# Optimization experiments

Hardware: AMD Instinct MI355X
Metric: run time of the kernel (lower is better)

Reference implementation:

```python
import jax, jax.numpy as jnp
import numpy as np

D_MODEL = 1024
N_HEADS = 16
D_K = D_MODEL // N_HEADS


def rotate_half(x):
    x1, x2 = x[..., : x.shape[-1] // 2], x[..., x.shape[-1] // 2:]
    return jnp.concatenate((-x2, x1), axis=-1)


def rope_cos_sin(seq_len, d_k, dtype):
    inv_freq = 1.0 / (10000.0 ** (jnp.arange(0, d_k, 2, dtype=jnp.float32) / d_k))
    t = jnp.arange(seq_len, dtype=jnp.float32)
    freqs = jnp.outer(t, inv_freq)            # [S, d_k/2]
    emb = jnp.concatenate((freqs, freqs), -1) # [S, d_k]
    return jnp.cos(emb).astype(dtype), jnp.sin(emb).astype(dtype)


def setup_inputs() -> dict:
    key = jax.random.key(0)
    ks = jax.random.split(key, 8)
    B, S = 1, 2048
    q = jax.random.normal(ks[0], (B, S, D_MODEL), jnp.float32)
    k = jax.random.normal(ks[1], (B, S, D_MODEL), jnp.float32)
    v = jax.random.normal(ks[2], (B, S, D_MODEL), jnp.float32)
    # xavier-uniform-ish weights for [d_model, d_model]
    bound = float(np.sqrt(6.0 / (D_MODEL + D_MODEL)))
    def W(kk):
        return jax.random.uniform(kk, (D_MODEL, D_MODEL), jnp.float32, -bound, bound)
    return {
        "query": q, "key": k, "value": v,
        "w_q": W(ks[3]), "w_k": W(ks[4]), "w_v": W(ks[5]),
        "w_o": W(ks[6]), "b_o": jnp.zeros((D_MODEL,), jnp.float32),
    }


def reference(query, key, value, w_q, w_k, w_v, w_o, b_o):
    B, Sq, _ = query.shape
    Sk = key.shape[1]
    # projections (torch Linear: x @ W.T)
    Q = (query @ w_q.T).reshape(B, Sq, N_HEADS, D_K).transpose(0, 2, 1, 3)
    K = (key @ w_k.T).reshape(B, Sk, N_HEADS, D_K).transpose(0, 2, 1, 3)
    V = (value @ w_v.T).reshape(B, Sk, N_HEADS, D_K).transpose(0, 2, 1, 3)
    # RoPE on Q and K (over head dim d_k)
    cos_q, sin_q = rope_cos_sin(Sq, D_K, Q.dtype)
    cos_k, sin_k = (cos_q, sin_q) if Sk == Sq else rope_cos_sin(Sk, D_K, K.dtype)
    Q = Q * cos_q + rotate_half(Q) * sin_q
    K = K * cos_k + rotate_half(K) * sin_k
    scores = jnp.einsum("bhqd,bhkd->bhqk", Q, K) / jnp.sqrt(jnp.float32(D_K)).astype(Q.dtype)
    attn = jax.nn.softmax(scores, axis=-1)          # [B,H,Sq,Sk]
    ctx = jnp.einsum("bhqk,bhkd->bhqd", attn, V)    # [B,H,Sq,d_k]
    ctx = ctx.transpose(0, 2, 1, 3).reshape(B, Sq, D_MODEL)
    out = ctx @ w_o.T + b_o
    return out, attn
```

## Files before the change

### kernel.cpp

```cpp
#include <hip/hip_runtime.h>
#include <hip/hip_bf16.h>

using short8 = __attribute__((ext_vector_type(8))) short;
using f32x4  = __attribute__((ext_vector_type(4))) float;

#define SEQ   2048
#define DM    1024
#define NHEAD 16
#define MB    1048576

#define GLD16(GP, LP) __builtin_amdgcn_global_load_lds(                      \
    (const __attribute__((address_space(1))) void*)(GP),                     \
    (__attribute__((address_space(3))) void*)(LP), 16, 0, 0)

static __device__ __forceinline__ short f2bf(float f) {
    union { __hip_bfloat16 b; short s; } u;
    u.b = __float2bfloat16(f);
    return u.s;
}
static __device__ __forceinline__ f32x4 mfma_bf16(short8 a, short8 b, f32x4 c) {
    return __builtin_amdgcn_mfma_f32_16x16x32_bf16(a, b, c, 0, 0, 0);
}

__global__ __launch_bounds__(256) void prep_kernel(
    const float* __restrict__ q, const float* __restrict__ k, const float* __restrict__ v,
    const float* __restrict__ wq, const float* __restrict__ wk, const float* __restrict__ wv,
    const float* __restrict__ wo, short* __restrict__ bf,
    float* __restrict__ cosT, float* __restrict__ sinT)
{
    long t = (long)blockIdx.x * 256 + threadIdx.x;
    if (t < 1310720) {
        long e0 = t * 8;
        const float* src; long off;
        if      (e0 < 2L*MB) { src = q;  off = e0; }
        else if (e0 < 4L*MB) { src = k;  off = e0 - 2L*MB; }
        else if (e0 < 6L*MB) { src = v;  off = e0 - 4L*MB; }
        else if (e0 < 7L*MB) { src = wq; off = e0 - 6L*MB; }
        else if (e0 < 8L*MB) { src = wk; off = e0 - 7L*MB; }
        else if (e0 < 9L*MB) { src = wv; off = e0 - 8L*MB; }
        else                 { src = wo; off = e0 - 9L*MB; }
        float4 a = *(const float4*)(src + off);
        float4 b = *(const float4*)(src + off + 4);
        short8 o;
        o[0]=f2bf(a.x); o[1]=f2bf(a.y); o[2]=f2bf(a.z); o[3]=f2bf(a.w);
        o[4]=f2bf(b.x); o[5]=f2bf(b.y); o[6]=f2bf(b.z); o[7]=f2bf(b.w);
        *(short8*)(bf + e0) = o;
    } else {
        long tt = t - 1310720;
        int s = (int)(tt >> 5), j = (int)(tt & 31);
        float invf = __expf(-(float)j * (9.210340371976184f / 32.0f));
        float arg = (float)s * invf;
        cosT[tt] = cosf(arg);
        sinT[tt] = sinf(arg);
    }
}

__global__ __launch_bounds__(256, 2) void gemm_qkv(
    short* __restrict__ wsbf, const float* __restrict__ cosT,
    const float* __restrict__ sinT)
{
    __shared__ short As[128 * 64];
    __shared__ short Bs[128 * 64];
    const int tid  = threadIdx.x;
    const int lane = tid & 63;
    const int wave = tid >> 6;
    const int q4   = lane >> 4;
    const int l16  = lane & 15;
    const int wm   = wave >> 1;
    const int wn   = wave & 1;
    const int m0   = blockIdx.y * 128;
    const int n0   = blockIdx.x * 128;
    const int z    = blockIdx.z;

    const short* A = wsbf + (size_t)z * (2*MB);
    const short* W = wsbf + 6*(size_t)MB + (size_t)z * MB;

    f32x4 zero = {0.f, 0.f, 0.f, 0.f};
    f32x4 acc[4][4];
    #pragma unroll
    for (int i = 0; i < 4; ++i)
        #pragma unroll
        for (int j = 0; j < 4; ++j) acc[i][j] = zero;

    const int r8 = tid >> 3, c8 = tid & 7;

    for (int k0 = 0; k0 < 1024; k0 += 64) {
        __syncthreads();
        #pragma unroll
        for (int r = 0; r < 4; ++r) {
            int row = r*32 + r8;
            int sw  = c8 ^ (row & 7);
            GLD16(A + (size_t)(m0+row)*1024 + k0 + sw*8, &As[(r*256 + tid)*8]);
            GLD16(W + (size_t)(n0+row)*1024 + k0 + sw*8, &Bs[(r*256 + tid)*8]);
        }
        __syncthreads();
        #pragma unroll
        for (int kk = 0; kk < 2; ++kk) {
            short8 af[4], bfr[4];
            #pragma unroll
            for (int i = 0; i < 4; ++i) {
                int ra = wm*64 + i*16 + l16;
                af[i]  = *(const short8*)&As[ra*64 + (((kk*4+q4) ^ (ra&7))*8)];
                int rb = wn*64 + i*16 + l16;
                bfr[i] = *(const short8*)&Bs[rb*64 + (((kk*4+q4) ^ (rb&7))*8)];
            }
            #pragma unroll
            for (int i = 0; i < 4; ++i)
                #pragma unroll
                for (int j = 0; j < 4; ++j)
                    acc[i][j] = mfma_bf16(af[i], bfr[j], acc[i][j]);
        }
    }

    const int h = (n0 >> 6) + wn;
    if (z < 2) {
        short* dst = wsbf + (size_t)(10 + 2*z) * MB;
        #pragma unroll
        for (int i = 0; i < 4; ++i) {
            #pragma unroll
            for (int jj = 0; jj < 4; ++jj) {
                int s = m0 + wm*64 + i*16 + q4*4 + jj;
                float c0 = cosT[(s<<5) + l16],      s0 = sinT[(s<<5) + l16];
                float c1 = cosT[(s<<5) + 16 + l16], s1 = sinT[(s<<5) + 16 + l16];
                float v0 = acc[i][0][jj], v1 = acc[i][1][jj];
                float v2 = acc[i][2][jj], v3 = acc[i][3][jj];
                size_t base = ((size_t)h*SEQ + s)*64;
                dst[base + l16]      = f2bf(v0*c0 - v2*s0);
                dst[base + 16 + l16] = f2bf(v1*c1 - v3*s1);
                dst[base + 32 + l16] = f2bf(v2*c0 + v0*s0);
                dst[base + 48 + l16] = f2bf(v3*c1 + v1*s1);
            }
        }
    } else {
        short* dst = wsbf + (size_t)14 * MB;
        #pragma unroll
        for (int i = 0; i < 4; ++i)
            #pragma unroll
            for (int j = 0; j < 4; ++j)
                #pragma unroll
                for (int jj = 0; jj < 4; ++jj) {
                    int s = m0 + wm*64 + i*16 + q4*4 + jj;
                    int d = j*16 + l16;
                    dst[((size_t)h*64 + d)*SEQ + s] = f2bf(acc[i][j][jj]);
                }
    }
}

__global__ __launch_bounds__(256, 2) void attn_kernel(
    const short* __restrict__ wsbf, short* __restrict__ ctxout,
    float* __restrict__ attn)
{
    __shared__ short Qs[64 * 64];
    __shared__ short Ks[2][128 * 64];
    __shared__ short Vs[64 * 128];
    __shared__ short Ps[4][16 * 128];
    const int tid = threadIdx.x, lane = tid & 63, wave = tid >> 6;
    const int q4 = lane >> 4, l16 = lane & 15;
    const int h = blockIdx.y, qt0 = blockIdx.x * 64;
    const short* Qg = wsbf + (size_t)10*MB + ((size_t)h*SEQ + qt0)*64;
    const short* Kg = wsbf + (size_t)12*MB + (size_t)h*SEQ*64;
    const short* Vg = wsbf + (size_t)14*MB + (size_t)h*64*SEQ;

    const int r8  = tid >> 3, c8  = tid & 7;
    const int r16 = tid >> 4, c16 = tid & 15;

    auto stageK = [&](int kt, short* buf) {
        #pragma unroll
        for (int r = 0; r < 4; ++r) {
            int row = r*32 + r8;
            int sw  = c8 ^ (row & 7);
            GLD16(Kg + (size_t)(kt*128 + row)*64 + sw*8, buf + (r*256 + tid)*8);
        }
    };
    auto stageV = [&](int kt) {
        #pragma unroll
        for (int r = 0; r < 4; ++r) {
            int row = r*16 + r16;
            int sw  = c16 ^ (row & 7);
            GLD16(Vg + (size_t)row*SEQ + kt*128 + sw*8, &Vs[(r*256 + tid)*8]);
        }
    };

    #pragma unroll
    for (int r = 0; r < 2; ++r) {
        int row = r*32 + r8;
        int sw  = c8 ^ (row & 7);
        GLD16(Qg + (size_t)row*64 + sw*8, &Qs[(r*256 + tid)*8]);
    }
    stageK(0, Ks[0]);
    __syncthreads();

    const int ra = wave*16 + l16;
    short8 a_q[2];
    #pragma unroll
    for (int kk = 0; kk < 2; ++kk)
        a_q[kk] = *(const short8*)&Qs[ra*64 + (((kk*4+q4) ^ (ra&7))*8)];

    f32x4 zero = {0.f, 0.f, 0.f, 0.f};
    f32x4 ctx[4] = {zero, zero, zero, zero};
    float rs[4] = {0.f, 0.f, 0.f, 0.f};
    const int frw = ((l16 & 7) + 2*(l16 >> 3)) & 7;

    for (int kt = 0; kt < 16; ++kt) {
        const short* Kb = (kt & 1) ? Ks[1] : Ks[0];
        short*       Kn = (kt & 1) ? Ks[0] : Ks[1];
        stageV(kt);
        if (kt < 15) stageK(kt + 1, Kn);
        #pragma unroll
        for (int nt = 0; nt < 8; ++nt) {
            f32x4 acc = zero;
            #pragma unroll
            for (int kk = 0; kk < 2; ++kk) {
                int rb = nt*16 + l16;
                short8 b = *(const short8*)&Kb[rb*64 + (((kk*4+q4) ^ (rb&7))*8)];
                acc = mfma_bf16(a_q[kk], b, acc);
            }
            #pragma unroll
            for (int jj = 0; jj < 4; ++jj) {
                float p = __expf(acc[jj] * 0.125f);
                rs[jj] += p;
                int prow = q4*4 + jj;
                int col  = nt*16 + l16;
                int fr   = ((prow & 7) + 2*(prow >> 3)) & 7;
                int phys = (col >> 3) ^ fr;
                Ps[wave][prow*128 + phys*8 + (col & 7)] = f2bf(p);
            }
        }
        if (kt < 15) asm volatile("s_waitcnt vmcnt(4) lgkmcnt(0)" ::: "memory");
        else         asm volatile("s_waitcnt vmcnt(0) lgkmcnt(0)" ::: "memory");
        __builtin_amdgcn_s_barrier();
        #pragma unroll
        for (int kks = 0; kks < 4; ++kks) {
            short8 a = *(const short8*)&Ps[wave][l16*128 + (((kks*4+q4) ^ frw)*8)];
            #pragma unroll
            for (int dt = 0; dt < 4; ++dt) {
                int rv = dt*16 + l16;
                short8 b = *(const short8*)&Vs[rv*128 + (((kks*4+q4) ^ (rv&7))*8)];
                ctx[dt] = mfma_bf16(a, b, ctx[dt]);
            }
        }
        asm volatile("s_waitcnt vmcnt(0) lgkmcnt(0)" ::: "memory");
        __builtin_amdgcn_s_barrier();
    }

    #pragma unroll
    for (int jj = 0; jj < 4; ++jj)
        #pragma unroll
        for (int m = 1; m < 16; m <<= 1)
            rs[jj] += __shfl_xor(rs[jj], m);
    float irs[4];
    #pragma unroll
    for (int jj = 0; jj < 4; ++jj) irs[jj] = 1.0f / rs[jj];

    const int qbase = qt0 + wave*16 + q4*4;
    #pragma unroll
    for (int dt = 0; dt < 4; ++dt)
        #pragma unroll
        for (int jj = 0; jj < 4; ++jj)
            ctxout[(size_t)(qbase + jj)*1024 + h*64 + dt*16 + l16] = f2bf(ctx[dt][jj] * irs[jj]);

    stageK(0, Ks[0]);
    asm volatile("s_waitcnt vmcnt(0) lgkmcnt(0)" ::: "memory");
    __builtin_amdgcn_s_barrier();

    float* arow = attn + (size_t)h*SEQ*SEQ;
    for (int kt = 0; kt < 16; ++kt) {
        const short* Kb = (kt & 1) ? Ks[1] : Ks[0];
        short*       Kn = (kt & 1) ? Ks[0] : Ks[1];
        if (kt < 15) stageK(kt + 1, Kn);
        #pragma unroll
        for (int nt = 0; nt < 8; ++nt) {
            f32x4 acc = zero;
            #pragma unroll
            for (int kk = 0; kk < 2; ++kk) {
                int rb = nt*16 + l16;
                short8 b = *(const short8*)&Kb[rb*64 + (((kk*4+q4) ^ (rb&7))*8)];
                acc = mfma_bf16(a_q[kk], b, acc);
            }
            #pragma unroll
            for (int jj = 0; jj < 4; ++jj)
                arow[(size_t)(qbase + jj)*SEQ + kt*128 + nt*16 + l16] =
                    __expf(acc[jj] * 0.125f) * irs[jj];
        }
        asm volatile("s_waitcnt vmcnt(32) lgkmcnt(0)" ::: "memory");
        __builtin_amdgcn_s_barrier();
    }
}

__global__ __launch_bounds__(256, 2) void gemm_out(
    const short* __restrict__ wsbf, const float* __restrict__ bo,
    float* __restrict__ out)
{
    __shared__ short As[128 * 64];
    __shared__ short Bs[64 * 64];
    const int tid = threadIdx.x, lane = tid & 63, wave = tid >> 6;
    const int q4 = lane >> 4, l16 = lane & 15;
    const int m0 = blockIdx.y * 128, n0 = blockIdx.x * 64;
    const short* A = wsbf + 16*(size_t)MB;
    const short* W = wsbf + 9*(size_t)MB;

    f32x4 zero = {0.f, 0.f, 0.f, 0.f};
    f32x4 acc[2][4];
    #pragma unroll
    for (int i = 0; i < 2; ++i)
        #pragma unroll
        for (int j = 0; j < 4; ++j) acc[i][j] = zero;

    const int r8 = tid >> 3, c8 = tid & 7;

    for (int k0 = 0; k0 < 1024; k0 += 64) {
        __syncthreads();
        #pragma unroll
        for (int r = 0; r < 4; ++r) {
            int row = r*32 + r8;
            int sw  = c8 ^ (row & 7);
            GLD16(A + (size_t)(m0+row)*1024 + k0 + sw*8, &As[(r*256 + tid)*8]);
        }
        #pragma unroll
        for (int r = 0; r < 2; ++r) {
            int row = r*32 + r8;
            int sw  = c8 ^ (row & 7);
            GLD16(W + (size_t)(n0+row)*1024 + k0 + sw*8, &Bs[(r*256 + tid)*8]);
        }
        __syncthreads();
        #pragma unroll
        for (int kk = 0; kk < 2; ++kk) {
            short8 af[2], bfr[4];
            #pragma unroll
            for (int i = 0; i < 2; ++i) {
                int ra = wave*32 + i*16 + l16;
                af[i] = *(const short8*)&As[ra*64 + (((kk*4+q4) ^ (ra&7))*8)];
            }
            #pragma unroll
            for (int j = 0; j < 4; ++j) {
                int rb = j*16 + l16;
                bfr[j] = *(const short8*)&Bs[rb*64 + (((kk*4+q4) ^ (rb&7))*8)];
            }
            #pragma unroll
            for (int i = 0; i < 2; ++i)
                #pragma unroll
                for (int j = 0; j < 4; ++j)
                    acc[i][j] = mfma_bf16(af[i], bfr[j], acc[i][j]);
        }
    }

    #pragma unroll
    for (int i = 0; i < 2; ++i)
        #pragma unroll
        for (int j = 0; j < 4; ++j)
            #pragma unroll
            for (int jj = 0; jj < 4; ++jj) {
                int gr = m0 + wave*32 + i*16 + q4*4 + jj;
                int gc = n0 + j*16 + l16;
                out[(size_t)gr*1024 + gc] = acc[i][j][jj] + bo[gc];
            }
}

extern "C" void kernel_launch(void* const* d_in, const int* in_sizes, int n_in,
                              void* d_out, int out_size, void* d_ws, size_t ws_size,
                              hipStream_t stream)
{
    const float* q  = (const float*)d_in[0];
    const float* k  = (const float*)d_in[1];
    const float* v  = (const float*)d_in[2];
    const float* wq = (const float*)d_in[3];
    const float* wk = (const float*)d_in[4];
    const float* wv = (const float*)d_in[5];
    const float* wo = (const float*)d_in[6];
    const float* bo = (const float*)d_in[7];

    short* wsbf = (short*)d_ws;
    float* cosT = (float*)((char*)d_ws + (size_t)36*MB);
    float* sinT = cosT + 65536;
    float* out  = (float*)d_out;
    float* attn = out + (size_t)SEQ*DM;

    hipLaunchKernelGGL(prep_kernel, dim3(5376), dim3(256), 0, stream,
                       q, k, v, wq, wk, wv, wo, wsbf, cosT, sinT);
    hipLaunchKernelGGL(gemm_qkv, dim3(8, 16, 3), dim3(256), 0, stream,
                       wsbf, cosT, sinT);
    hipLaunchKernelGGL(attn_kernel, dim3(32, 16), dim3(256), 0, stream,
                       wsbf, wsbf + (size_t)16*MB, attn);
    hipLaunchKernelGGL(gemm_out, dim3(16, 16), dim3(256), 0, stream,
                       wsbf, bo, out);
}
```

Before: 410.4 us.

## Double-buffer GEMM k-loops, keep P in registers, and vectorize attention-row stores

Both projection GEMMs now double-buffer their LDS tiles so the next k-slice loads while MFMAs run on the current one. The attention kernel swaps the MFMA operand order so each lane holds a transposed score tile. That lets the bf16 P fragments be packed straight from registers instead of round-tripping through an LDS scratch buffer, with V stored in a matching permuted sequence order. The attention-probability writeout becomes float4 stores per lane, and row sums are reduced with fewer shuffles. The cost is double the LDS in the GEMMs, which may reduce occupancy, plus more register pressure from holding P in the attention kernel.

New measurement: 389.2 us. -5.2%, faster.

```diff
diff --git a/kernel.cpp b/kernel.cpp
--- a/kernel.cpp
+++ b/kernel.cpp
@@ -59,8 +59,8 @@
     short* __restrict__ wsbf, const float* __restrict__ cosT,
     const float* __restrict__ sinT)
 {
-    __shared__ short As[128 * 64];
-    __shared__ short Bs[128 * 64];
+    __shared__ short As[2][128 * 64];
+    __shared__ short Bs[2][128 * 64];
     const int tid  = threadIdx.x;
     const int lane = tid & 63;
     const int wave = tid >> 6;
@@ -84,25 +84,33 @@
 
     const int r8 = tid >> 3, c8 = tid & 7;
 
-    for (int k0 = 0; k0 < 1024; k0 += 64) {
-        __syncthreads();
+    auto stage = [&](int k0, int buf) {
         #pragma unroll
         for (int r = 0; r < 4; ++r) {
             int row = r*32 + r8;
             int sw  = c8 ^ (row & 7);
-            GLD16(A + (size_t)(m0+row)*1024 + k0 + sw*8, &As[(r*256 + tid)*8]);
-            GLD16(W + (size_t)(n0+row)*1024 + k0 + sw*8, &Bs[(r*256 + tid)*8]);
-        }
-        __syncthreads();
+            GLD16(A + (size_t)(m0+row)*1024 + k0 + sw*8, &As[buf][(r*256 + tid)*8]);
+            GLD16(W + (size_t)(n0+row)*1024 + k0 + sw*8, &Bs[buf][(r*256 + tid)*8]);
+        }
+    };
+
+    stage(0, 0);
+    for (int t = 0; t < 16; ++t) {
+        if (t < 15) stage((t+1)*64, (t+1)&1);
+        if (t < 15) asm volatile("s_waitcnt vmcnt(8)" ::: "memory");
+        else        asm volatile("s_waitcnt vmcnt(0)" ::: "memory");
+        asm volatile("s_barrier" ::: "memory");
+        const short* as = As[t&1];
+        const short* bs = Bs[t&1];
         #pragma unroll
         for (int kk = 0; kk < 2; ++kk) {
             short8 af[4], bfr[4];
             #pragma unroll
             for (int i = 0; i < 4; ++i) {
                 int ra = wm*64 + i*16 + l16;
-                af[i]  = *(const short8*)&As[ra*64 + (((kk*4+q4) ^ (ra&7))*8)];
+                af[i]  = *(const short8*)&as[ra*64 + (((kk*4+q4) ^ (ra&7))*8)];
                 int rb = wn*64 + i*16 + l16;
-                bfr[i] = *(const short8*)&Bs[rb*64 + (((kk*4+q4) ^ (rb&7))*8)];
+                bfr[i] = *(const short8*)&bs[rb*64 + (((kk*4+q4) ^ (rb&7))*8)];
             }
             #pragma unroll
             for (int i = 0; i < 4; ++i)
@@ -110,6 +118,7 @@
                 for (int j = 0; j < 4; ++j)
                     acc[i][j] = mfma_bf16(af[i], bfr[j], acc[i][j]);
         }
+        asm volatile("s_barrier" ::: "memory");
     }
 
     const int h = (n0 >> 6) + wn;
@@ -139,9 +148,10 @@
             for (int j = 0; j < 4; ++j)
                 #pragma unroll
                 for (int jj = 0; jj < 4; ++jj) {
-                    int s = m0 + wm*64 + i*16 + q4*4 + jj;
-                    int d = j*16 + l16;
-                    dst[((size_t)h*64 + d)*SEQ + s] = f2bf(acc[i][j][jj]);
+                    int s  = m0 + wm*64 + i*16 + q4*4 + jj;
+                    int sp = (s & ~31) + q4*8 + (i&1)*4 + jj;
+                    int d  = j*16 + l16;
+                    dst[((size_t)h*64 + d)*SEQ + sp] = f2bf(acc[i][j][jj]);
                 }
     }
 }
@@ -153,7 +163,6 @@
     __shared__ short Qs[64 * 64];
     __shared__ short Ks[2][128 * 64];
     __shared__ short Vs[64 * 128];
-    __shared__ short Ps[4][16 * 128];
     const int tid = threadIdx.x, lane = tid & 63, wave = tid >> 6;
     const int q4 = lane >> 4, l16 = lane & 15;
     const int h = blockIdx.y, qt0 = blockIdx.x * 64;
@@ -198,14 +207,14 @@
 
     f32x4 zero = {0.f, 0.f, 0.f, 0.f};
     f32x4 ctx[4] = {zero, zero, zero, zero};
-    float rs[4] = {0.f, 0.f, 0.f, 0.f};
-    const int frw = ((l16 & 7) + 2*(l16 >> 3)) & 7;
+    float rsl = 0.f;
 
     for (int kt = 0; kt < 16; ++kt) {
         const short* Kb = (kt & 1) ? Ks[1] : Ks[0];
         short*       Kn = (kt & 1) ? Ks[0] : Ks[1];
         stageV(kt);
         if (kt < 15) stageK(kt + 1, Kn);
+        float p[8][4];
         #pragma unroll
         for (int nt = 0; nt < 8; ++nt) {
             f32x4 acc = zero;
@@ -213,44 +222,45 @@
             for (int kk = 0; kk < 2; ++kk) {
                 int rb = nt*16 + l16;
                 short8 b = *(const short8*)&Kb[rb*64 + (((kk*4+q4) ^ (rb&7))*8)];
-                acc = mfma_bf16(a_q[kk], b, acc);
+                acc = mfma_bf16(b, a_q[kk], acc);
             }
             #pragma unroll
             for (int jj = 0; jj < 4; ++jj) {
-                float p = __expf(acc[jj] * 0.125f);
-                rs[jj] += p;
-                int prow = q4*4 + jj;
-                int col  = nt*16 + l16;
-                int fr   = ((prow & 7) + 2*(prow >> 3)) & 7;
-                int phys = (col >> 3) ^ fr;
-                Ps[wave][prow*128 + phys*8 + (col & 7)] = f2bf(p);
-            }
-        }
-        if (kt < 15) asm volatile("s_waitcnt vmcnt(4) lgkmcnt(0)" ::: "memory");
-        else         asm volatile("s_waitcnt vmcnt(0) lgkmcnt(0)" ::: "memory");
-        __builtin_amdgcn_s_barrier();
-        #pragma unroll
-        for (int kks = 0; kks < 4; ++kks) {
-            short8 a = *(const short8*)&Ps[wave][l16*128 + (((kks*4+q4) ^ frw)*8)];
+                float pv = __expf(acc[jj] * 0.125f);
+                rsl += pv;
+                p[nt][jj] = pv;
+            }
+        }
+        short8 pa[4];
+        #pragma unroll
+        for (int w = 0; w < 4; ++w) {
+            #pragma unroll
+            for (int j = 0; j < 4; ++j) { pa[w][j] = f2bf(p[2*w][j]); pa[w][4+j] = f2bf(p[2*w+1][j]); }
+        }
+        if (kt < 15) asm volatile("s_waitcnt vmcnt(4)" ::: "memory");
+        else         asm volatile("s_waitcnt vmcnt(0)" ::: "memory");
+        asm volatile("s_barrier" ::: "memory");
+        __builtin_amdgcn_s_setprio(1);
+        #pragma unroll
+        for (int w = 0; w < 4; ++w) {
             #pragma unroll
             for (int dt = 0; dt < 4; ++dt) {
                 int rv = dt*16 + l16;
-                short8 b = *(const short8*)&Vs[rv*128 + (((kks*4+q4) ^ (rv&7))*8)];
-                ctx[dt] = mfma_bf16(a, b, ctx[dt]);
-            }
-        }
+                short8 b = *(const short8*)&Vs[rv*128 + (((w*4+q4) ^ (rv&7))*8)];
+                ctx[dt] = mfma_bf16(pa[w], b, ctx[dt]);
+            }
+        }
+        __builtin_amdgcn_s_setprio(0);
         asm volatile("s_waitcnt vmcnt(0) lgkmcnt(0)" ::: "memory");
-        __builtin_amdgcn_s_barrier();
-    }
-
-    #pragma unroll
-    for (int jj = 0; jj < 4; ++jj)
-        #pragma unroll
-        for (int m = 1; m < 16; m <<= 1)
-            rs[jj] += __shfl_xor(rs[jj], m);
+        asm volatile("s_barrier" ::: "memory");
+    }
+
+    rsl += __shfl_xor(rsl, 16);
+    rsl += __shfl_xor(rsl, 32);
+    float irs_l = 1.0f / rsl;
     float irs[4];
     #pragma unroll
-    for (int jj = 0; jj < 4; ++jj) irs[jj] = 1.0f / rs[jj];
+    for (int jj = 0; jj < 4; ++jj) irs[jj] = __shfl(irs_l, q4*4 + jj);
 
     const int qbase = qt0 + wave*16 + q4*4;
     #pragma unroll
@@ -260,10 +270,10 @@
             ctxout[(size_t)(qbase + jj)*1024 + h*64 + dt*16 + l16] = f2bf(ctx[dt][jj] * irs[jj]);
 
     stageK(0, Ks[0]);
-    asm volatile("s_waitcnt vmcnt(0) lgkmcnt(0)" ::: "memory");
-    __builtin_amdgcn_s_barrier();
-
-    float* arow = attn + (size_t)h*SEQ*SEQ;
+    asm volatile("s_waitcnt vmcnt(0)" ::: "memory");
+    asm volatile("s_barrier" ::: "memory");
+
+    float* arow = attn + (size_t)h*SEQ*SEQ + (size_t)(qt0 + wave*16 + l16)*SEQ;
     for (int kt = 0; kt < 16; ++kt) {
         const short* Kb = (kt & 1) ? Ks[1] : Ks[0];
         short*       Kn = (kt & 1) ? Ks[0] : Ks[1];
@@ -275,15 +285,17 @@
             for (int kk = 0; kk < 2; ++kk) {
                 int rb = nt*16 + l16;
                 short8 b = *(const short8*)&Kb[rb*64 + (((kk*4+q4) ^ (rb&7))*8)];
-                acc = mfma_bf16(a_q[kk], b, acc);
-            }
-            #pragma unroll
-            for (int jj = 0; jj < 4; ++jj)
-                arow[(size_t)(qbase + jj)*SEQ + kt*128 + nt*16 + l16] =
-                    __expf(acc[jj] * 0.125f) * irs[jj];
-        }
-        asm volatile("s_waitcnt vmcnt(32) lgkmcnt(0)" ::: "memory");
-        __builtin_amdgcn_s_barrier();
+                acc = mfma_bf16(b, a_q[kk], acc);
+            }
+            float4 o;
+            o.x = __expf(acc[0] * 0.125f) * irs_l;
+            o.y = __expf(acc[1] * 0.125f) * irs_l;
+            o.z = __expf(acc[2] * 0.125f) * irs_l;
+            o.w = __expf(acc[3] * 0.125f) * irs_l;
+            *(float4*)&arow[kt*128 + nt*16 + q4*4] = o;
+        }
+        asm volatile("s_waitcnt vmcnt(8) lgkmcnt(0)" ::: "memory");
+        asm volatile("s_barrier" ::: "memory");
     }
 }
 
@@ -291,8 +303,8 @@
     const short* __restrict__ wsbf, const float* __restrict__ bo,
     float* __restrict__ out)
 {
-    __shared__ short As[128 * 64];
-    __shared__ short Bs[64 * 64];
+    __shared__ short As[2][128 * 64];
+    __shared__ short Bs[2][64 * 64];
     const int tid = threadIdx.x, lane = tid & 63, wave = tid >> 6;
     const int q4 = lane >> 4, l16 = lane & 15;
     const int m0 = blockIdx.y * 128, n0 = blockIdx.x * 64;
@@ -308,33 +320,41 @@
 
     const int r8 = tid >> 3, c8 = tid & 7;
 
-    for (int k0 = 0; k0 < 1024; k0 += 64) {
-        __syncthreads();
+    auto stage = [&](int k0, int buf) {
         #pragma unroll
         for (int r = 0; r < 4; ++r) {
             int row = r*32 + r8;
             int sw  = c8 ^ (row & 7);
-            GLD16(A + (size_t)(m0+row)*1024 + k0 + sw*8, &As[(r*256 + tid)*8]);
+            GLD16(A + (size_t)(m0+row)*1024 + k0 + sw*8, &As[buf][(r*256 + tid)*8]);
         }
         #pragma unroll
         for (int r = 0; r < 2; ++r) {
             int row = r*32 + r8;
             int sw  = c8 ^ (row & 7);
-            GLD16(W + (size_t)(n0+row)*1024 + k0 + sw*8, &Bs[(r*256 + tid)*8]);
-        }
-        __syncthreads();
+            GLD16(W + (size_t)(n0+row)*1024 + k0 + sw*8, &Bs[buf][(r*256 + tid)*8]);
+        }
+    };
+
+    stage(0, 0);
+    for (int t = 0; t < 16; ++t) {
+        if (t < 15) stage((t+1)*64, (t+1)&1);
+        if (t < 15) asm volatile("s_waitcnt vmcnt(6)" ::: "memory");
+        else        asm volatile("s_waitcnt vmcnt(0)" ::: "memory");
+        asm volatile("s_barrier" ::: "memory");
+        const short* as = As[t&1];
+        const short* bs = Bs[t&1];
         #pragma unroll
         for (int kk = 0; kk < 2; ++kk) {
             short8 af[2], bfr[4];
             #pragma unroll
             for (int i = 0; i < 2; ++i) {
                 int ra = wave*32 + i*16 + l16;
-                af[i] = *(const short8*)&As[ra*64 + (((kk*4+q4) ^ (ra&7))*8)];
+                af[i] = *(const short8*)&as[ra*64 + (((kk*4+q4) ^ (ra&7))*8)];
             }
             #pragma unroll
             for (int j = 0; j < 4; ++j) {
                 int rb = j*16 + l16;
-                bfr[j] = *(const short8*)&Bs[rb*64 + (((kk*4+q4) ^ (rb&7))*8)];
+                bfr[j] = *(const short8*)&bs[rb*64 + (((kk*4+q4) ^ (rb&7))*8)];
             }
             #pragma unroll
             for (int i = 0; i < 2; ++i)
@@ -342,6 +362,7 @@
                 for (int j = 0; j < 4; ++j)
                     acc[i][j] = mfma_bf16(af[i], bfr[j], acc[i][j]);
         }
+        asm volatile("s_barrier" ::: "memory");
     }
 
     #pragma unroll
```
